# Kernel tuning notes

Hardware: AMD Instinct MI355X
Metric: run time of the kernel (lower is better)

Reference implementation:

```python
import jax, jax.numpy as jnp
import numpy as np

N = 50000
D = 64
E = 800000


def setup_inputs() -> dict:
    key = jax.random.key(0)
    ks = jax.random.split(key, 8)
    x = jax.random.normal(ks[0], (N, D), dtype=jnp.float32)
    edge_index = jax.random.randint(ks[1], (2, E), 0, N, dtype=jnp.int64)
    edge_attr = jax.random.normal(ks[2], (E,), dtype=jnp.float32)
    x_agg_emb = jax.random.normal(ks[3], (N, D), dtype=jnp.float32)
    # Linear(2D -> D) weights stored as [in, out]; scale ~ kaiming-ish
    W_msg = jax.random.normal(ks[4], (2 * D, D), dtype=jnp.float32) * (1.0 / np.sqrt(2 * D))
    b_msg = jnp.zeros((D,), dtype=jnp.float32)
    W_upd = jax.random.normal(ks[5], (2 * D, D), dtype=jnp.float32) * (1.0 / np.sqrt(2 * D))
    b_upd = jnp.zeros((D,), dtype=jnp.float32)
    return {"x": x, "edge_index": edge_index, "edge_attr": edge_attr,
            "x_agg_emb": x_agg_emb, "W_msg": W_msg, "b_msg": b_msg,
            "W_upd": W_upd, "b_upd": b_upd}


def reference(x, edge_index, edge_attr, x_agg_emb, W_msg, b_msg, W_upd, b_upd):
    col, row = edge_index[0], edge_index[1]
    # edge-weighted gather: [E, D]
    msgs = edge_attr[:, None] * x[col]
    # scatter-mean over destination nodes (dim_size = N)
    summed = jax.ops.segment_sum(msgs, row, num_segments=N)            # [N, D]
    counts = jax.ops.segment_sum(jnp.ones_like(edge_attr), row, num_segments=N)  # [N]
    x_agg = summed / jnp.maximum(counts, 1.0)[:, None]
    # message MLP: Linear(2D->D) + ReLU
    m = jax.nn.relu(jnp.concatenate([x_agg, x_agg_emb], axis=-1) @ W_msg + b_msg)
    # update MLP: Linear(2D->D) + ReLU
    out = jax.nn.relu(jnp.concatenate([x, m], axis=-1) @ W_upd + b_upd)
    return out
```

## Files before the change

kernel.cpp:

```cpp
#include <hip/hip_runtime.h>


#define CAP 48
#define FILLB 2048

typedef __attribute__((ext_vector_type(8))) short short8;
typedef __attribute__((ext_vector_type(4))) float f32x4;

__device__ __forceinline__ unsigned short f2bf(float f) {
    unsigned int u = __float_as_uint(f);
    u += 0x7FFFu + ((u >> 16) & 1u);
    return (unsigned short)(u >> 16);
}
__device__ __forceinline__ float bf2f(unsigned short h) {
    return __uint_as_float((unsigned)h << 16);
}
__device__ __forceinline__ uint4 pack8(const float* v) {
    uint4 r;
    r.x = (unsigned)f2bf(v[0]) | ((unsigned)f2bf(v[1]) << 16);
    r.y = (unsigned)f2bf(v[2]) | ((unsigned)f2bf(v[3]) << 16);
    r.z = (unsigned)f2bf(v[4]) | ((unsigned)f2bf(v[5]) << 16);
    r.w = (unsigned)f2bf(v[6]) | ((unsigned)f2bf(v[7]) << 16);
    return r;
}

__global__ __launch_bounds__(256) void zero_f32(float* p, int n) {
    int i = blockIdx.x * 256 + threadIdx.x;
    if (i < n) p[i] = 0.0f;
}
__global__ __launch_bounds__(256) void zero_i32(int* p, int n) {
    int i = blockIdx.x * 256 + threadIdx.x;
    if (i < n) p[i] = 0;
}

__global__ __launch_bounds__(256) void cvt_zero(
    const float* __restrict__ x, unsigned short* __restrict__ xh,
    int* __restrict__ cnt, int N)
{
    int id = blockIdx.x * 256 + threadIdx.x;
    if (id < N * 8) {
        const float* src = x + (size_t)id * 8;
        float4 p0 = ((const float4*)src)[0];
        float4 p1 = ((const float4*)src)[1];
        float v[8];
        v[0] = p0.x; v[1] = p0.y; v[2] = p0.z; v[3] = p0.w;
        v[4] = p1.x; v[5] = p1.y; v[6] = p1.z; v[7] = p1.w;
        *(uint4*)&xh[(size_t)id * 8] = pack8(v);
    }
    if (id < N) cnt[id] = 0;
}

__global__ __launch_bounds__(256) void fill_group_kernel(
    const int* __restrict__ ei, const float* __restrict__ ea,
    int* cnt, int2* __restrict__ packed, int E, int N)
{
    const int g   = blockIdx.x & 7;
    const int bg  = blockIdx.x >> 3;
    const int nb  = gridDim.x >> 3;
    const int rpg = (N + 7) >> 3;
    const int rlo = g * rpg;
    const int rhi = min(rlo + rpg, N);
    const int chunk = (E + nb - 1) / nb;
    const int lo = bg * chunk;
    const int hi = min(lo + chunk, E);
    int e = lo + (int)threadIdx.x;
    for (; e + 768 < hi; e += 1024) {
        int r0 = ei[E + e];
        int r1 = ei[E + e + 256];
        int r2 = ei[E + e + 512];
        int r3 = ei[E + e + 768];
        int c0 = ei[e], c1 = ei[e + 256], c2 = ei[e + 512], c3 = ei[e + 768];
        float a0 = ea[e], a1 = ea[e + 256], a2 = ea[e + 512], a3 = ea[e + 768];
        bool m0 = (r0 >= rlo) & (r0 < rhi);
        bool m1 = (r1 >= rlo) & (r1 < rhi);
        bool m2 = (r2 >= rlo) & (r2 < rhi);
        bool m3 = (r3 >= rlo) & (r3 < rhi);
        int p0 = CAP, p1 = CAP, p2 = CAP, p3 = CAP;
        if (m0) p0 = atomicAdd(&cnt[r0], 1);
        if (m1) p1 = atomicAdd(&cnt[r1], 1);
        if (m2) p2 = atomicAdd(&cnt[r2], 1);
        if (m3) p3 = atomicAdd(&cnt[r3], 1);
        if (m0 && p0 < CAP) packed[(size_t)r0 * CAP + p0] = make_int2(c0, __float_as_int(a0));
        if (m1 && p1 < CAP) packed[(size_t)r1 * CAP + p1] = make_int2(c1, __float_as_int(a1));
        if (m2 && p2 < CAP) packed[(size_t)r2 * CAP + p2] = make_int2(c2, __float_as_int(a2));
        if (m3 && p3 < CAP) packed[(size_t)r3 * CAP + p3] = make_int2(c3, __float_as_int(a3));
    }
    for (; e < hi; e += 256) {
        int row = ei[E + e];
        if (row >= rlo && row < rhi) {
            int pos = atomicAdd(&cnt[row], 1);
            if (pos < CAP)
                packed[(size_t)row * CAP + pos] = make_int2(ei[e], __float_as_int(ea[e]));
        }
    }
}


__device__ __forceinline__ void stage_W1024(
    unsigned short* Wb, const float* Wg, int t)
{
    int R = t >> 6, nn = t & 63;
    int kt = R >> 2, qq = R & 3;
    const float* src = Wg + (size_t)(kt * 32 + qq * 8) * 64 + nn;
    float v[8];
    #pragma unroll
    for (int j = 0; j < 8; j++) v[j] = src[(size_t)j * 64];
    *(uint4*)&Wb[R * 528 + nn * 8] = pack8(v);
}

__global__ __launch_bounds__(1024) void gather_mlp(
    const int2* __restrict__ packed, const int* __restrict__ cnt,
    const unsigned short* __restrict__ xh, const float* __restrict__ emb,
    const float* __restrict__ Wm, const float* __restrict__ bm,
    const float* __restrict__ Wu, const float* __restrict__ bu,
    float* __restrict__ out, int N)
{
    __shared__ __align__(16) unsigned short Ab [64 * 128];
    __shared__ __align__(16) unsigned short Ab2[64 * 128];
    __shared__ __align__(16) unsigned short Wb [16 * 528];
    __shared__ __align__(16) unsigned short Wb2[16 * 528];

    const int t    = threadIdx.x;
    const int g    = blockIdx.x & 7;
    const int tile = blockIdx.x >> 3;
    const int rpg  = (N + 7) >> 3;
    const int rlo  = g * rpg;
    const int rhi  = min(rlo + rpg, N);
    const int tile0 = rlo + tile * 64;
    const int w    = t >> 6;
    const int lane = t & 63;
    const int q = lane >> 4, ln = lane & 15;

    stage_W1024(Wb,  Wm, t);
    stage_W1024(Wb2, Wu, t);
    if (t < 512) {
        int r = t >> 3, c = t & 7;
        int node = tile0 + r;
        uint4 d = make_uint4(0u, 0u, 0u, 0u);
        if (node < rhi)
            d = *(const uint4*)&xh[(size_t)node * 64 + c * 8];
        *(uint4*)&Ab2[r * 128 + ((c ^ (r & 15)) * 8)] = d;
    } else {
        int s = t - 512;
        int r = s >> 3, c = s & 7;
        int node = tile0 + r;
        float v[8] = {0.f, 0.f, 0.f, 0.f, 0.f, 0.f, 0.f, 0.f};
        if (node < rhi) {
            const float* src = emb + (size_t)node * 64 + c * 8;
            float4 p0 = ((const float4*)src)[0];
            float4 p1 = ((const float4*)src)[1];
            v[0] = p0.x; v[1] = p0.y; v[2] = p0.z; v[3] = p0.w;
            v[4] = p1.x; v[5] = p1.y; v[6] = p1.z; v[7] = p1.w;
        }
        int ch = 8 + c;
        *(uint4*)&Ab[r * 128 + ((ch ^ (r & 15)) * 8)] = pack8(v);
    }

    const int wu = __builtin_amdgcn_readfirstlane(w);
    int nodec[4], degv[4], dlv[4];
    #pragma unroll
    for (int i = 0; i < 4; i++) {
        int node = tile0 + wu * 4 + i;
        bool ok = node < rhi;
        nodec[i] = ok ? node : rlo;
        degv[i]  = ok ? cnt[node] : 0;
        dlv[i]   = min(degv[i], CAP);
    }
    int maxdl = max(max(dlv[0], dlv[1]), max(dlv[2], dlv[3]));
    float ac[4][4];
    #pragma unroll
    for (int i = 0; i < 4; i++) {
        #pragma unroll
        for (int k = 0; k < 4; k++) ac[i][k] = 0.f;
    }

    for (int j = 0; j < maxdl; j += 8) {
        int   colm[4][8];
        float attm[4][8];
        #pragma unroll
        for (int i = 0; i < 4; i++) {
            const int4* s4 = (const int4*)(packed + (size_t)nodec[i] * CAP);
            #pragma unroll
            for (int m = 0; m < 4; m++) {
                int4 d = s4[(j >> 1) + m];
                int e0 = j + 2 * m;
                colm[i][2 * m]     = max(0, min(d.x, N - 1));
                colm[i][2 * m + 1] = max(0, min(d.z, N - 1));
                attm[i][2 * m]     = (e0     < dlv[i]) ? __int_as_float(d.y) : 0.f;
                attm[i][2 * m + 1] = (e0 + 1 < dlv[i]) ? __int_as_float(d.w) : 0.f;
            }
        }
        unsigned short us[4][8];
        #pragma unroll
        for (int i = 0; i < 4; i++) {
            #pragma unroll
            for (int k = 0; k < 8; k++)
                us[i][k] = xh[((unsigned)colm[i][k] << 6) | lane];
        }
        #pragma unroll
        for (int i = 0; i < 4; i++) {
            #pragma unroll
            for (int k = 0; k < 8; k++)
                ac[i][k & 3] += attm[i][k] * bf2f(us[i][k]);
        }
    }
    #pragma unroll
    for (int i = 0; i < 4; i++) {
        int r = wu * 4 + i;
        float mean = ((ac[i][0] + ac[i][1]) + (ac[i][2] + ac[i][3]))
                     / fmaxf((float)degv[i], 1.0f);
        int ch = lane >> 3;
        Ab[r * 128 + ((ch ^ (r & 15)) * 8) + (lane & 7)] = f2bf(mean);
    }
    __syncthreads();

    const int wr = w & 3, wn = w >> 2;
    f32x4 acc = (f32x4){0.f, 0.f, 0.f, 0.f};
    {
        const int rr = wr * 16 + ln;
        #pragma unroll
        for (int kt = 0; kt < 4; kt++) {
            short8 af = *(const short8*)&Ab[rr * 128 + (((kt * 4 + q) ^ ln) * 8)];
            short8 bf = *(const short8*)&Wb[(kt * 4 + q) * 528 + (wn * 16 + ln) * 8];
            acc = __builtin_amdgcn_mfma_f32_16x16x32_bf16(af, bf, acc, 0, 0, 0);
        }
    }

    {
        float bmv = bm[wn * 16 + ln];
        #pragma unroll
        for (int reg = 0; reg < 4; reg++) {
            float mv = fmaxf(acc[reg] + bmv, 0.f);
            int rr = wr * 16 + q * 4 + reg;
            int k  = 64 + wn * 16 + ln;
            int ch = k >> 3;
            Ab2[rr * 128 + ((ch ^ (rr & 15)) * 8) + (k & 7)] = f2bf(mv);
        }
    }
    __syncthreads();

    f32x4 acc2 = (f32x4){0.f, 0.f, 0.f, 0.f};
    {
        const int rr = wr * 16 + ln;
        #pragma unroll
        for (int kt = 0; kt < 4; kt++) {
            short8 af = *(const short8*)&Ab2[rr * 128 + (((kt * 4 + q) ^ ln) * 8)];
            short8 bf = *(const short8*)&Wb2[(kt * 4 + q) * 528 + (wn * 16 + ln) * 8];
            acc2 = __builtin_amdgcn_mfma_f32_16x16x32_bf16(af, bf, acc2, 0, 0, 0);
        }
    }
    {
        float buv = bu[wn * 16 + ln];
        #pragma unroll
        for (int reg = 0; reg < 4; reg++) {
            int rr = wr * 16 + q * 4 + reg;
            int node = tile0 + rr;
            if (node < rhi)
                out[(size_t)node * 64 + wn * 16 + ln] =
                    fmaxf(acc2[reg] + buv, 0.f);
        }
    }
}


__global__ __launch_bounds__(256) void hist_kernel(
    const int* __restrict__ ei, int* hist, int E)
{
    int e = blockIdx.x * 256 + threadIdx.x;
    if (e < E) atomicAdd(&hist[ei[E + e]], 1);
}
__global__ __launch_bounds__(256) void scan_partial_kernel(
    const int* __restrict__ hist, int* partial, int N)
{
    __shared__ int s[256];
    int t = threadIdx.x;
    int i = blockIdx.x * 256 + t;
    s[t] = (i < N) ? hist[i] : 0;
    __syncthreads();
    #pragma unroll
    for (int off = 128; off > 0; off >>= 1) {
        if (t < off) s[t] += s[t + off];
        __syncthreads();
    }
    if (t == 0) partial[blockIdx.x] = s[0];
}
__global__ __launch_bounds__(256) void scan_top_kernel(
    const int* __restrict__ partial, int* scanP, int NB)
{
    __shared__ int s[256];
    int t = threadIdx.x;
    int v = (t < NB) ? partial[t] : 0;
    s[t] = v;
    __syncthreads();
    #pragma unroll
    for (int off = 1; off < 256; off <<= 1) {
        int add = (t >= off) ? s[t - off] : 0;
        __syncthreads();
        s[t] += add;
        __syncthreads();
    }
    if (t < NB) scanP[t] = s[t] - v;
}
__global__ __launch_bounds__(256) void scan_final_kernel(
    const int* __restrict__ hist, const int* __restrict__ scanP,
    int* offsets, int* cursor, int N)
{
    __shared__ int s[256];
    int t = threadIdx.x;
    int i = blockIdx.x * 256 + t;
    int v = (i < N) ? hist[i] : 0;
    s[t] = v;
    __syncthreads();
    #pragma unroll
    for (int off = 1; off < 256; off <<= 1) {
        int add = (t >= off) ? s[t - off] : 0;
        __syncthreads();
        s[t] += add;
        __syncthreads();
    }
    if (i < N) {
        int o = scanP[blockIdx.x] + s[t] - v;
        offsets[i] = o;
        cursor[i]  = o;
    }
}
__global__ __launch_bounds__(256) void fill_kernel(
    const int* __restrict__ ei, const float* __restrict__ ea,
    int* cursor, int2* __restrict__ packed, int E)
{
    int e = blockIdx.x * 256 + threadIdx.x;
    if (e >= E) return;
    int pos = atomicAdd(&cursor[ei[E + e]], 1);
    packed[pos] = make_int2(ei[e], __float_as_int(ea[e]));
}
__global__ __launch_bounds__(256) void gather_kernel(
    const int2* __restrict__ packed, const int* __restrict__ offsets,
    const int* __restrict__ hist, const float* __restrict__ x,
    float* __restrict__ out, int N)
{
    int t = threadIdx.x;
    int n = blockIdx.x * 4 + (t >> 6);
    int lane = t & 63;
    if (n >= N) return;
    int start = offsets[n];
    int deg   = hist[n];
    float a0 = 0.f, a1 = 0.f, a2 = 0.f, a3 = 0.f;
    int j = 0;
    for (; j + 4 <= deg; j += 4) {
        int2 p0 = packed[start + j];
        int2 p1 = packed[start + j + 1];
        int2 p2 = packed[start + j + 2];
        int2 p3 = packed[start + j + 3];
        a0 += __int_as_float(p0.y) * x[(size_t)p0.x * 64 + lane];
        a1 += __int_as_float(p1.y) * x[(size_t)p1.x * 64 + lane];
        a2 += __int_as_float(p2.y) * x[(size_t)p2.x * 64 + lane];
        a3 += __int_as_float(p3.y) * x[(size_t)p3.x * 64 + lane];
    }
    for (; j < deg; j++) {
        int2 p = packed[start + j];
        a0 += __int_as_float(p.y) * x[(size_t)p.x * 64 + lane];
    }
    float acc = (a0 + a1) + (a2 + a3);
    out[(size_t)n * 64 + lane] = acc / fmaxf((float)deg, 1.0f);
}


__global__ __launch_bounds__(256) void scatter_kernel(
    const int* __restrict__ ei, const float* __restrict__ ea,
    const float* __restrict__ x, float* summed, float* counts, int E)
{
    int idx = blockIdx.x * 256 + threadIdx.x;
    int e = idx >> 6;
    int d = idx & 63;
    if (e >= E) return;
    float v = ea[e] * x[(size_t)ei[e] * 64 + d];
    atomicAdd(&summed[(size_t)ei[E + e] * 64 + d], v);
    if (d == 0) atomicAdd(&counts[ei[E + e]], 1.0f);
}


__device__ __forceinline__ void stage_W(
    unsigned short* Wb, const float* Wg, int t)
{
    #pragma unroll
    for (int c = t; c < 1024; c += 256) {
        int R = c >> 6, nn = c & 63;
        int kt = R >> 2, qq = R & 3;
        const float* src = Wg + (size_t)(kt * 32 + qq * 8) * 64 + nn;
        float v[8];
        #pragma unroll
        for (int j = 0; j < 8; j++) v[j] = src[(size_t)j * 64];
        *(uint4*)&Wb[R * 528 + nn * 8] = pack8(v);
    }
}

__device__ __forceinline__ void mfma_tile(
    const unsigned short* Ab, const unsigned short* Wb,
    int wv, int lane, f32x4 acc[4])
{
    const int q  = lane >> 4;
    const int ln = lane & 15;
    const int rr = wv * 16 + ln;
    short8 af[4];
    #pragma unroll
    for (int kt = 0; kt < 4; kt++)
        af[kt] = *(const short8*)&Ab[rr * 128 + (((kt * 4 + q) ^ ln) * 8)];
    #pragma unroll
    for (int nt = 0; nt < 4; nt++) {
        #pragma unroll
        for (int kt = 0; kt < 4; kt++) {
            short8 bf = *(const short8*)&Wb[(kt * 4 + q) * 528 + (nt * 16 + ln) * 8];
            acc[nt] = __builtin_amdgcn_mfma_f32_16x16x32_bf16(af[kt], bf, acc[nt], 0, 0, 0);
        }
    }
}

__global__ __launch_bounds__(256) void mfma_mlp(
    const float* Aagg, const float* __restrict__ Aemb,
    const float* __restrict__ counts, const float* __restrict__ Xin,
    const float* __restrict__ Wm, const float* __restrict__ bm,
    const float* __restrict__ Wu, const float* __restrict__ bu,
    float* out, int N)
{
    __shared__ __align__(16) unsigned short Ab[64 * 128];
    __shared__ __align__(16) unsigned short Wb[16 * 528];

    const int t = threadIdx.x;
    const int tile0 = blockIdx.x * 64;
    const int lane = t & 63, wv = t >> 6;
    const int q = lane >> 4, ln = lane & 15;

    stage_W(Wb, Wm, t);
    #pragma unroll
    for (int s = t; s < 1024; s += 256) {
        int r = s >> 4, chunk = s & 15;
        int node = tile0 + r;
        float v[8] = {0.f, 0.f, 0.f, 0.f, 0.f, 0.f, 0.f, 0.f};
        if (node < N) {
            const float* src = (chunk < 8)
                ? (Aagg + (size_t)node * 64 + chunk * 8)
                : (Aemb + (size_t)node * 64 + (chunk - 8) * 8);
            float4 p0 = ((const float4*)src)[0];
            float4 p1 = ((const float4*)src)[1];
            v[0] = p0.x; v[1] = p0.y; v[2] = p0.z; v[3] = p0.w;
            v[4] = p1.x; v[5] = p1.y; v[6] = p1.z; v[7] = p1.w;
            if (counts && chunk < 8) {
                float rc = 1.0f / fmaxf(counts[node], 1.0f);
                #pragma unroll
                for (int i = 0; i < 8; i++) v[i] *= rc;
            }
        }
        *(uint4*)&Ab[r * 128 + ((chunk ^ (r & 15)) * 8)] = pack8(v);
    }
    __syncthreads();

    f32x4 acc[4];
    #pragma unroll
    for (int nt = 0; nt < 4; nt++) acc[nt] = (f32x4){0.f, 0.f, 0.f, 0.f};
    mfma_tile(Ab, Wb, wv, lane, acc);
    __syncthreads();

    stage_W(Wb, Wu, t);
    #pragma unroll
    for (int s = t; s < 512; s += 256) {
        int r = s >> 3, chunk = s & 7;
        int node = tile0 + r;
        float v[8] = {0.f, 0.f, 0.f, 0.f, 0.f, 0.f, 0.f, 0.f};
        if (node < N) {
            const float* src = Xin + (size_t)node * 64 + chunk * 8;
            float4 p0 = ((const float4*)src)[0];
            float4 p1 = ((const float4*)src)[1];
            v[0] = p0.x; v[1] = p0.y; v[2] = p0.z; v[3] = p0.w;
            v[4] = p1.x; v[5] = p1.y; v[6] = p1.z; v[7] = p1.w;
        }
        *(uint4*)&Ab[r * 128 + ((chunk ^ (r & 15)) * 8)] = pack8(v);
    }
    #pragma unroll
    for (int nt = 0; nt < 4; nt++) {
        float bmv = bm[nt * 16 + ln];
        #pragma unroll
        for (int reg = 0; reg < 4; reg++) {
            float mv = fmaxf(acc[nt][reg] + bmv, 0.f);
            int rr = wv * 16 + q * 4 + reg;
            int k  = 64 + nt * 16 + ln;
            int ch = k >> 3;
            Ab[rr * 128 + ((ch ^ (rr & 15)) * 8) + (k & 7)] = f2bf(mv);
        }
    }
    __syncthreads();

    f32x4 acc2[4];
    #pragma unroll
    for (int nt = 0; nt < 4; nt++) acc2[nt] = (f32x4){0.f, 0.f, 0.f, 0.f};
    mfma_tile(Ab, Wb, wv, lane, acc2);
    #pragma unroll
    for (int nt = 0; nt < 4; nt++) {
        float buv = bu[nt * 16 + ln];
        #pragma unroll
        for (int reg = 0; reg < 4; reg++) {
            int rr = wv * 16 + q * 4 + reg;
            int node = tile0 + rr;
            if (node < N)
                out[(size_t)node * 64 + nt * 16 + ln] =
                    fmaxf(acc2[nt][reg] + buv, 0.f);
        }
    }
}

extern "C" void kernel_launch(void* const* d_in, const int* in_sizes, int n_in,
                              void* d_out, int out_size, void* d_ws, size_t ws_size,
                              hipStream_t stream) {
    const float* x   = (const float*)d_in[0];
    const int*   ei  = (const int*)d_in[1];
    const float* ea  = (const float*)d_in[2];
    const float* emb = (const float*)d_in[3];
    const float* Wm  = (const float*)d_in[4];
    const float* bm  = (const float*)d_in[5];
    const float* Wu  = (const float*)d_in[6];
    const float* bu  = (const float*)d_in[7];
    float*       out = (float*)d_out;

    const int N = in_sizes[0] / 64;
    const int E = in_sizes[2];
    const int NB = (N + 255) / 256;

    const int eblocks = (E + 255) / 256;
    const int mblocks = (N + 63) / 64;
    const int rpg = (N + 7) / 8;

    const size_t need_cap = (size_t)N * CAP * 8 + (size_t)N * 128 + (size_t)N * 4;
    const size_t need_csr = (size_t)E * 8 + ((size_t)3 * N + 512) * 4;

    if (ws_size >= need_cap) {
        char* ws = (char*)d_ws;
        int2*           packed = (int2*)ws;
        unsigned short* xh     = (unsigned short*)(ws + (size_t)N * CAP * 8);
        int*            cnt    = (int*)(ws + (size_t)N * CAP * 8 + (size_t)N * 128);

        int cb = (N * 8 + 255) / 256;
        cvt_zero<<<cb, 256, 0, stream>>>(x, xh, cnt, N);
        fill_group_kernel<<<FILLB, 256, 0, stream>>>(ei, ea, cnt, packed, E, N);
        int tpg = (rpg + 63) / 64;
        gather_mlp<<<8 * tpg, 1024, 0, stream>>>(packed, cnt, xh, emb,
                                                 Wm, bm, Wu, bu, out, N);
    } else if (ws_size >= need_csr && NB <= 256) {
        char* ws = (char*)d_ws;
        int2* packed  = (int2*)ws;
        int*  hist    = (int*)(ws + (size_t)E * 8);
        int*  offsets = hist + N;
        int*  cursor  = offsets + N;
        int*  partial = cursor + N;
        int*  scanP   = partial + 256;

        zero_i32<<<NB, 256, 0, stream>>>(hist, N);
        hist_kernel<<<eblocks, 256, 0, stream>>>(ei, hist, E);
        scan_partial_kernel<<<NB, 256, 0, stream>>>(hist, partial, N);
        scan_top_kernel<<<1, 256, 0, stream>>>(partial, scanP, NB);
        scan_final_kernel<<<NB, 256, 0, stream>>>(hist, scanP, offsets, cursor, N);
        fill_kernel<<<eblocks, 256, 0, stream>>>(ei, ea, cursor, packed, E);
        gather_kernel<<<(N + 3) / 4, 256, 0, stream>>>(packed, offsets, hist, x, out, N);
        mfma_mlp<<<mblocks, 256, 0, stream>>>(out, emb, nullptr, x,
                                              Wm, bm, Wu, bu, out, N);
    } else {
        float* counts = (float*)d_ws;
        zero_f32<<<(N * 64 + 255) / 256, 256, 0, stream>>>(out, N * 64);
        zero_f32<<<NB, 256, 0, stream>>>(counts, N);
        long long total = (long long)E * 64;
        scatter_kernel<<<(int)((total + 255) / 256), 256, 0, stream>>>(
            ei, ea, x, out, counts, E);
        mfma_mlp<<<mblocks, 256, 0, stream>>>(out, emb, counts, x,
                                              Wm, bm, Wu, bu, out, N);
    }
}
```

Before: 161.2 us.

## Halve gather block size, prefetch packed edges, zero-fill slots to drop masking

```diff
diff --git a/kernel.cpp b/kernel.cpp
--- a/kernel.cpp
+++ b/kernel.cpp
@@ -35,9 +35,10 @@
 
 __global__ __launch_bounds__(256) void cvt_zero(
     const float* __restrict__ x, unsigned short* __restrict__ xh,
-    int* __restrict__ cnt, int N)
+    int* __restrict__ cnt, uint4* __restrict__ pk4, int N)
 {
     int id = blockIdx.x * 256 + threadIdx.x;
+    int nthreads = gridDim.x * 256;
     if (id < N * 8) {
         const float* src = x + (size_t)id * 8;
         float4 p0 = ((const float4*)src)[0];
@@ -48,6 +49,9 @@
         *(uint4*)&xh[(size_t)id * 8] = pack8(v);
     }
     if (id < N) cnt[id] = 0;
+    const uint4 z = make_uint4(0u, 0u, 0u, 0u);
+    for (size_t k = id; k < (size_t)N * (CAP / 2); k += nthreads)
+        pk4[k] = z;
 }
 
 __global__ __launch_bounds__(256) void fill_group_kernel(
@@ -96,19 +100,39 @@
 }
 
 
-__device__ __forceinline__ void stage_W1024(
+__device__ __forceinline__ void stage_W512(
     unsigned short* Wb, const float* Wg, int t)
 {
-    int R = t >> 6, nn = t & 63;
-    int kt = R >> 2, qq = R & 3;
-    const float* src = Wg + (size_t)(kt * 32 + qq * 8) * 64 + nn;
-    float v[8];
-    #pragma unroll
-    for (int j = 0; j < 8; j++) v[j] = src[(size_t)j * 64];
-    *(uint4*)&Wb[R * 528 + nn * 8] = pack8(v);
-}
-
-__global__ __launch_bounds__(1024) void gather_mlp(
+    #pragma unroll
+    for (int c = t; c < 1024; c += 512) {
+        int R = c >> 6, nn = c & 63;
+        int kt = R >> 2, qq = R & 3;
+        const float* src = Wg + (size_t)(kt * 32 + qq * 8) * 64 + nn;
+        float v[8];
+        #pragma unroll
+        for (int j = 0; j < 8; j++) v[j] = src[(size_t)j * 64];
+        *(uint4*)&Wb[R * 528 + nn * 8] = pack8(v);
+    }
+}
+
+#define CONSUME(D)                                                          \
+    {                                                                       \
+        unsigned short u0[8], u1[8];                                        \
+        _Pragma("unroll")                                                   \
+        for (int n = 0; n < 8; n++) {                                       \
+            unsigned v0 = ((unsigned)D[n].x << 7) + lane2;                  \
+            unsigned v1 = ((unsigned)D[n].z << 7) + lane2;                  \
+            u0[n] = *(const unsigned short*)((const char*)xh + v0);         \
+            u1[n] = *(const unsigned short*)((const char*)xh + v1);         \
+        }                                                                   \
+        _Pragma("unroll")                                                   \
+        for (int n = 0; n < 8; n++) {                                       \
+            ac0[n] += __int_as_float(D[n].y) * bf2f(u0[n]);                 \
+            ac1[n] += __int_as_float(D[n].w) * bf2f(u1[n]);                 \
+        }                                                                   \
+    }
+
+__global__ __launch_bounds__(512) void gather_mlp(
     const int2* __restrict__ packed, const int* __restrict__ cnt,
     const unsigned short* __restrict__ xh, const float* __restrict__ emb,
     const float* __restrict__ Wm, const float* __restrict__ bm,
@@ -127,22 +151,23 @@
     const int rlo  = g * rpg;
     const int rhi  = min(rlo + rpg, N);
     const int tile0 = rlo + tile * 64;
-    const int w    = t >> 6;
     const int lane = t & 63;
     const int q = lane >> 4, ln = lane & 15;
-
-    stage_W1024(Wb,  Wm, t);
-    stage_W1024(Wb2, Wu, t);
-    if (t < 512) {
+    const unsigned lane2 = (unsigned)lane * 2;
+    const int wu = __builtin_amdgcn_readfirstlane(t >> 6);
+
+    stage_W512(Wb,  Wm, t);
+    stage_W512(Wb2, Wu, t);
+    {
         int r = t >> 3, c = t & 7;
         int node = tile0 + r;
         uint4 d = make_uint4(0u, 0u, 0u, 0u);
         if (node < rhi)
             d = *(const uint4*)&xh[(size_t)node * 64 + c * 8];
         *(uint4*)&Ab2[r * 128 + ((c ^ (r & 15)) * 8)] = d;
-    } else {
-        int s = t - 512;
-        int r = s >> 3, c = s & 7;
+    }
+    {
+        int r = t >> 3, c = t & 7;
         int node = tile0 + r;
         float v[8] = {0.f, 0.f, 0.f, 0.f, 0.f, 0.f, 0.f, 0.f};
         if (node < rhi) {
@@ -156,108 +181,114 @@
         *(uint4*)&Ab[r * 128 + ((ch ^ (r & 15)) * 8)] = pack8(v);
     }
 
-    const int wu = __builtin_amdgcn_readfirstlane(w);
-    int nodec[4], degv[4], dlv[4];
-    #pragma unroll
-    for (int i = 0; i < 4; i++) {
-        int node = tile0 + wu * 4 + i;
+    const int4* s4 = (const int4*)packed;
+    int seg[8], deg[8];
+    int maxdl = 0;
+    #pragma unroll
+    for (int n = 0; n < 8; n++) {
+        int node = tile0 + wu * 8 + n;
         bool ok = node < rhi;
-        nodec[i] = ok ? node : rlo;
-        degv[i]  = ok ? cnt[node] : 0;
-        dlv[i]   = min(degv[i], CAP);
-    }
-    int maxdl = max(max(dlv[0], dlv[1]), max(dlv[2], dlv[3]));
-    float ac[4][4];
-    #pragma unroll
-    for (int i = 0; i < 4; i++) {
-        #pragma unroll
-        for (int k = 0; k < 4; k++) ac[i][k] = 0.f;
-    }
-
-    for (int j = 0; j < maxdl; j += 8) {
-        int   colm[4][8];
-        float attm[4][8];
-        #pragma unroll
-        for (int i = 0; i < 4; i++) {
-            const int4* s4 = (const int4*)(packed + (size_t)nodec[i] * CAP);
-            #pragma unroll
-            for (int m = 0; m < 4; m++) {
-                int4 d = s4[(j >> 1) + m];
-                int e0 = j + 2 * m;
-                colm[i][2 * m]     = max(0, min(d.x, N - 1));
-                colm[i][2 * m + 1] = max(0, min(d.z, N - 1));
-                attm[i][2 * m]     = (e0     < dlv[i]) ? __int_as_float(d.y) : 0.f;
-                attm[i][2 * m + 1] = (e0 + 1 < dlv[i]) ? __int_as_float(d.w) : 0.f;
-            }
-        }
-        unsigned short us[4][8];
-        #pragma unroll
-        for (int i = 0; i < 4; i++) {
-            #pragma unroll
-            for (int k = 0; k < 8; k++)
-                us[i][k] = xh[((unsigned)colm[i][k] << 6) | lane];
-        }
-        #pragma unroll
-        for (int i = 0; i < 4; i++) {
-            #pragma unroll
-            for (int k = 0; k < 8; k++)
-                ac[i][k & 3] += attm[i][k] * bf2f(us[i][k]);
-        }
-    }
-    #pragma unroll
-    for (int i = 0; i < 4; i++) {
-        int r = wu * 4 + i;
-        float mean = ((ac[i][0] + ac[i][1]) + (ac[i][2] + ac[i][3]))
-                     / fmaxf((float)degv[i], 1.0f);
+        int nd = ok ? node : rlo;
+        seg[n] = nd * (CAP / 2);
+        deg[n] = ok ? cnt[node] : 0;
+        maxdl  = max(maxdl, ok ? min(deg[n], CAP) : 0);
+    }
+    float ac0[8], ac1[8];
+    #pragma unroll
+    for (int n = 0; n < 8; n++) { ac0[n] = 0.f; ac1[n] = 0.f; }
+
+    int maxb = (maxdl + 1) >> 1;
+    int4 dc[8], dn[8];
+    #pragma unroll
+    for (int n = 0; n < 8; n++) dc[n] = s4[seg[n]];
+    int jb = 0;
+    while (jb < maxb) {
+        int jn = min(jb + 1, CAP / 2 - 1);
+        #pragma unroll
+        for (int n = 0; n < 8; n++) dn[n] = s4[seg[n] + jn];
+        CONSUME(dc);
+        jb++;
+        if (jb >= maxb) break;
+        int jn2 = min(jb + 1, CAP / 2 - 1);
+        #pragma unroll
+        for (int n = 0; n < 8; n++) dc[n] = s4[seg[n] + jn2];
+        CONSUME(dn);
+        jb++;
+    }
+
+    #pragma unroll
+    for (int n = 0; n < 8; n++) {
+        int r = wu * 8 + n;
+        int node = tile0 + r;
+        float mean = (node < rhi)
+            ? (ac0[n] + ac1[n]) / fmaxf((float)deg[n], 1.0f) : 0.f;
         int ch = lane >> 3;
         Ab[r * 128 + ((ch ^ (r & 15)) * 8) + (lane & 7)] = f2bf(mean);
     }
     __syncthreads();
 
-    const int wr = w & 3, wn = w >> 2;
-    f32x4 acc = (f32x4){0.f, 0.f, 0.f, 0.f};
+    const int wr = wu & 3;
+    const int wn0 = (wu >> 2) * 2, wn1 = wn0 + 1;
+    f32x4 acc0 = (f32x4){0.f, 0.f, 0.f, 0.f};
+    f32x4 acc1 = (f32x4){0.f, 0.f, 0.f, 0.f};
     {
         const int rr = wr * 16 + ln;
         #pragma unroll
         for (int kt = 0; kt < 4; kt++) {
             short8 af = *(const short8*)&Ab[rr * 128 + (((kt * 4 + q) ^ ln) * 8)];
-            short8 bf = *(const short8*)&Wb[(kt * 4 + q) * 528 + (wn * 16 + ln) * 8];
-            acc = __builtin_amdgcn_mfma_f32_16x16x32_bf16(af, bf, acc, 0, 0, 0);
+            short8 bf0 = *(const short8*)&Wb[(kt * 4 + q) * 528 + (wn0 * 16 + ln) * 8];
+            short8 bf1 = *(const short8*)&Wb[(kt * 4 + q) * 528 + (wn1 * 16 + ln) * 8];
+            acc0 = __builtin_amdgcn_mfma_f32_16x16x32_bf16(af, bf0, acc0, 0, 0, 0);
+            acc1 = __builtin_amdgcn_mfma_f32_16x16x32_bf16(af, bf1, acc1, 0, 0, 0);
         }
     }
 
     {
-        float bmv = bm[wn * 16 + ln];
+        float bmv0 = bm[wn0 * 16 + ln];
+        float bmv1 = bm[wn1 * 16 + ln];
         #pragma unroll
         for (int reg = 0; reg < 4; reg++) {
-            float mv = fmaxf(acc[reg] + bmv, 0.f);
             int rr = wr * 16 + q * 4 + reg;
-            int k  = 64 + wn * 16 + ln;
-            int ch = k >> 3;
-            Ab2[rr * 128 + ((ch ^ (rr & 15)) * 8) + (k & 7)] = f2bf(mv);
-        }
-    }
-    __syncthreads();
-
-    f32x4 acc2 = (f32x4){0.f, 0.f, 0.f, 0.f};
+            {
+                float mv = fmaxf(acc0[reg] + bmv0, 0.f);
+                int k  = 64 + wn0 * 16 + ln;
+                int ch = k >> 3;
+                Ab2[rr * 128 + ((ch ^ (rr & 15)) * 8) + (k & 7)] = f2bf(mv);
+            }
+            {
+                float mv = fmaxf(acc1[reg] + bmv1, 0.f);
+                int k  = 64 + wn1 * 16 + ln;
+                int ch = k >> 3;
+                Ab2[rr * 128 + ((ch ^ (rr & 15)) * 8) + (k & 7)] = f2bf(mv);
+            }
+        }
+    }
+    __syncthreads();
+
+    f32x4 acc2a = (f32x4){0.f, 0.f, 0.f, 0.f};
+    f32x4 acc2b = (f32x4){0.f, 0.f, 0.f, 0.f};
     {
         const int rr = wr * 16 + ln;
         #pragma unroll
         for (int kt = 0; kt < 4; kt++) {
             short8 af = *(const short8*)&Ab2[rr * 128 + (((kt * 4 + q) ^ ln) * 8)];
-            short8 bf = *(const short8*)&Wb2[(kt * 4 + q) * 528 + (wn * 16 + ln) * 8];
-            acc2 = __builtin_amdgcn_mfma_f32_16x16x32_bf16(af, bf, acc2, 0, 0, 0);
+            short8 bf0 = *(const short8*)&Wb2[(kt * 4 + q) * 528 + (wn0 * 16 + ln) * 8];
+            short8 bf1 = *(const short8*)&Wb2[(kt * 4 + q) * 528 + (wn1 * 16 + ln) * 8];
+            acc2a = __builtin_amdgcn_mfma_f32_16x16x32_bf16(af, bf0, acc2a, 0, 0, 0);
+            acc2b = __builtin_amdgcn_mfma_f32_16x16x32_bf16(af, bf1, acc2b, 0, 0, 0);
         }
     }
     {
-        float buv = bu[wn * 16 + ln];
+        float buv0 = bu[wn0 * 16 + ln];
+        float buv1 = bu[wn1 * 16 + ln];
         #pragma unroll
         for (int reg = 0; reg < 4; reg++) {
             int rr = wr * 16 + q * 4 + reg;
             int node = tile0 + rr;
-            if (node < rhi)
-                out[(size_t)node * 64 + wn * 16 + ln] =
-                    fmaxf(acc2[reg] + buv, 0.f);
+            if (node < rhi) {
+                out[(size_t)node * 64 + wn0 * 16 + ln] = fmaxf(acc2a[reg] + buv0, 0.f);
+                out[(size_t)node * 64 + wn1 * 16 + ln] = fmaxf(acc2b[reg] + buv1, 0.f);
+            }
         }
     }
 }
@@ -538,11 +569,11 @@
         int*            cnt    = (int*)(ws + (size_t)N * CAP * 8 + (size_t)N * 128);
 
         int cb = (N * 8 + 255) / 256;
-        cvt_zero<<<cb, 256, 0, stream>>>(x, xh, cnt, N);
+        cvt_zero<<<cb, 256, 0, stream>>>(x, xh, cnt, (uint4*)packed, N);
         fill_group_kernel<<<FILLB, 256, 0, stream>>>(ei, ea, cnt, packed, E, N);
         int tpg = (rpg + 63) / 64;
-        gather_mlp<<<8 * tpg, 1024, 0, stream>>>(packed, cnt, xh, emb,
-                                                 Wm, bm, Wu, bu, out, N);
+        gather_mlp<<<8 * tpg, 512, 0, stream>>>(packed, cnt, xh, emb,
+                                                Wm, bm, Wu, bu, out, N);
     } else if (ws_size >= need_csr && NB <= 256) {
         char* ws = (char*)d_ws;
         int2* packed  = (int2*)ws;
```

Measured after the change: 163.7 us (median of 3 runs). About the same (+1.5%).
